# Performance work log

Measured on AMD Instinct MI355X. Metric: run time of the kernel, lower is better.

The kernel has to match this reference:

```python
import jax, jax.numpy as jnp
import numpy as np

# J2 (von Mises) plane-strain elastoplasticity with linear isotropic hardening
# (faithful stand-in for pyprnn's J2Material: elastic predictor + radial return,
#  committed history = plastic strain tensor + accumulated plastic strain).
E_MOD = 3130.0   # Young's modulus (epoxy, MPa)
NU = 0.37        # Poisson ratio
SIG_Y = 64.8     # initial yield stress
H_ISO = 300.0    # linear isotropic hardening modulus
MU = E_MOD / (2.0 * (1.0 + NU))
LAM = E_MOD * NU / ((1.0 + NU) * (1.0 - 2.0 * NU))


def j2_update(eps, eps_p, alpha):
    """eps: [P,3] (exx, eyy, gamma_xy engineering); eps_p: [P,4] (xx,yy,zz,xy tensorial);
    alpha: [P] accumulated plastic strain. Returns (stress [P,3], eps_p_new, alpha_new)."""
    ee_xx = eps[:, 0] - eps_p[:, 0]
    ee_yy = eps[:, 1] - eps_p[:, 1]
    ee_zz = -eps_p[:, 2]                      # plane strain: total ezz = 0
    ee_xy = 0.5 * eps[:, 2] - eps_p[:, 3]     # tensorial shear
    tr = ee_xx + ee_yy + ee_zz
    # trial (elastic predictor) stress
    sxx = LAM * tr + 2.0 * MU * ee_xx
    syy = LAM * tr + 2.0 * MU * ee_yy
    szz = LAM * tr + 2.0 * MU * ee_zz
    sxy = 2.0 * MU * ee_xy
    p = (sxx + syy + szz) / 3.0
    dxx, dyy, dzz = sxx - p, syy - p, szz - p
    q = jnp.sqrt(1.5 * (dxx * dxx + dyy * dyy + dzz * dzz + 2.0 * sxy * sxy))
    f = q - (SIG_Y + H_ISO * alpha)
    dgam = jnp.maximum(f, 0.0) / (3.0 * MU + H_ISO)   # radial return, closed form
    qs = jnp.maximum(q, 1e-12)
    nxx, nyy, nzz, nxy = 1.5 * dxx / qs, 1.5 * dyy / qs, 1.5 * dzz / qs, 1.5 * sxy / qs
    two_mu_dg = 2.0 * MU * dgam
    sig = jnp.stack([sxx - two_mu_dg * nxx, syy - two_mu_dg * nyy, sxy - two_mu_dg * nxy], axis=-1)
    eps_p_new = eps_p + dgam[:, None] * jnp.stack([nxx, nyy, nzz, nxy], axis=-1)
    alpha_new = alpha + dgam
    return sig, eps_p_new, alpha_new


def setup_inputs() -> dict:
    key = jax.random.key(0)
    k1, k2, k3 = jax.random.split(key, 3)
    B, T, F = 16384, 128, 3
    MATPTS = 16
    L, O = MATPTS * F, 3
    x = jax.random.normal(k1, (B, T, F), dtype=jnp.float32) * 0.02  # strain paths
    W1 = jax.random.normal(k2, (L, F), dtype=jnp.float32) * (1.0 / np.sqrt(F))
    W2 = jax.random.normal(k3, (O, L), dtype=jnp.float32) * (1.0 / np.sqrt(L))
    return {"x": x, "W1": W1, "W2": W2}


def reference(x, W1, W2):
    B, T, F = x.shape
    L = W1.shape[0]
    P = B * (L // F)                 # total material points = batch * mat_pts
    W2s = jax.nn.softplus(W2)        # SoftLayer: positive weights, no bias
    xt = jnp.swapaxes(x, 0, 1)       # [T, B, F]

    def step(carry, xi):
        eps_p, alpha = carry
        lat = xi @ W1.T                       # fc1 (no bias): [B, L]
        eps = lat.reshape(P, F)               # per-material-point strain
        sig, eps_p, alpha = j2_update(eps, eps_p, alpha)   # update + commit
        out = sig.reshape(B, L) @ W2s.T       # fc2 softplus-weighted linear
        return (eps_p, alpha), out

    carry0 = (jnp.zeros((P, 4), jnp.float32), jnp.zeros((P,), jnp.float32))
    _, ys = jax.lax.scan(step, carry0, xt)    # ys: [T, B, O]
    return jnp.swapaxes(ys, 0, 1)             # [B, T, O]
```

## Files before the change

kernel.cpp:

```cpp
#include <hip/hip_runtime.h>
#include <math.h>


#define BLOCK 256
#define BPB 32
#define TSTEPS 128
#define ROWF (TSTEPS * 3)
#define ROWP 388

typedef float v2 __attribute__((ext_vector_type(2)));

static __device__ __forceinline__ v2 vfma(v2 a, v2 b, v2 c) {
    return __builtin_elementwise_fma(a, b, c);
}
static __device__ __forceinline__ v2 vmax(v2 a, v2 b) {
    return __builtin_elementwise_max(a, b);
}

#define DPP_BFLY3(a, b, c)                                                       \
  asm volatile(                                                                  \
    "s_nop 1\n\t"                                                                \
    "v_add_f32_dpp %0, %0, %0 quad_perm:[1,0,3,2] row_mask:0xf bank_mask:0xf\n\t"\
    "v_add_f32_dpp %1, %1, %1 quad_perm:[1,0,3,2] row_mask:0xf bank_mask:0xf\n\t"\
    "v_add_f32_dpp %2, %2, %2 quad_perm:[1,0,3,2] row_mask:0xf bank_mask:0xf\n\t"\
    "v_add_f32_dpp %0, %0, %0 quad_perm:[2,3,0,1] row_mask:0xf bank_mask:0xf\n\t"\
    "v_add_f32_dpp %1, %1, %1 quad_perm:[2,3,0,1] row_mask:0xf bank_mask:0xf\n\t"\
    "v_add_f32_dpp %2, %2, %2 quad_perm:[2,3,0,1] row_mask:0xf bank_mask:0xf\n\t"\
    "v_add_f32_dpp %0, %0, %0 row_half_mirror row_mask:0xf bank_mask:0xf\n\t"    \
    "v_add_f32_dpp %1, %1, %1 row_half_mirror row_mask:0xf bank_mask:0xf\n\t"    \
    "v_add_f32_dpp %2, %2, %2 row_half_mirror row_mask:0xf bank_mask:0xf"        \
    : "+v"(a), "+v"(b), "+v"(c))

__global__ __launch_bounds__(BLOCK, 2)
void prnn_j2_kernel(const float* __restrict__ x,
                    const float* __restrict__ W1,
                    const float* __restrict__ W2,
                    float* __restrict__ out)
{
    constexpr float MU    = (float)(3130.0 / (2.0 * (1.0 + 0.37)));
    constexpr float LAM   = (float)(3130.0 * 0.37 / ((1.0 + 0.37) * (1.0 - 2.0 * 0.37)));
    constexpr float SIG_Y = 64.8f;
    constexpr float H_ISO = 300.0f;
    const float TWO_MU  = 2.0f * MU;
    const float K3MU    = 3.0f * MU;
    const float INV_DEN = 1.0f / (3.0f * MU + H_ISO);
    const float KBULK   = LAM + TWO_MU * (1.0f / 3.0f);
    const float C_Q2    = 6.0f * MU * MU;
    const v2 VTHIRD = {1.0f/3.0f, 1.0f/3.0f};
    const v2 VQMIN  = {1e-24f, 1e-24f};
    const v2 VZERO  = {0.0f, 0.0f};

    __shared__ float xs[BPB * ROWP + 12];

    const int tid = threadIdx.x;
    const int bl  = tid >> 3;
    const int l   = tid & 7;
    const int blockBase = blockIdx.x * (BPB * ROWF);

    {
        const float4* xg = (const float4*)(x + blockBase);
        for (int i4 = tid; i4 < BPB * ROWF / 4; i4 += BLOCK) {
            int b  = i4 / (ROWF / 4);
            int r4 = i4 - b * (ROWF / 4);
            ((float4*)(xs + b * ROWP))[r4] = xg[i4];
        }
    }

    const int pa = l, pb = l + 8;
    v2 w1p[3][3], w2p[3][3];
    #pragma unroll
    for (int c = 0; c < 3; ++c)
        #pragma unroll
        for (int f = 0; f < 3; ++f) {
            w1p[c][f].x = W1[(3 * pa + c) * 3 + f];
            w1p[c][f].y = W1[(3 * pb + c) * 3 + f];
        }
    #pragma unroll
    for (int o = 0; o < 3; ++o)
        #pragma unroll
        for (int c = 0; c < 3; ++c) {
            float wa = W2[o * 48 + 3 * pa + c];
            float wb = W2[o * 48 + 3 * pb + c];
            w2p[o][c].x = fmaxf(wa, 0.0f) + log1pf(expf(-fabsf(wa)));
            w2p[o][c].y = fmaxf(wb, 0.0f) + log1pf(expf(-fabsf(wb)));
        }

    __syncthreads();

    v2 p0 = VZERO, p1 = VZERO, p2 = VZERO, p3 = VZERO;
    v2 yld = {SIG_Y, SIG_Y};
    float* xrow = &xs[bl * ROWP];
    const float4* xv = (const float4*)xrow;

#define J2_STEP(x0_, x1_, x2_, wp_)                                          \
  {                                                                          \
    const float x0s = (x0_), x1s = (x1_), x2s = (x2_);                       \
    const v2 x0 = {x0s, x0s}, x1 = {x1s, x1s}, x2 = {x2s, x2s};              \
    const v2 e0 = vfma(w1p[0][0], x0, vfma(w1p[0][1], x1, w1p[0][2] * x2));  \
    const v2 e1 = vfma(w1p[1][0], x0, vfma(w1p[1][1], x1, w1p[1][2] * x2));  \
    const v2 e2 = vfma(w1p[2][0], x0, vfma(w1p[2][1], x1, w1p[2][2] * x2));  \
    const v2 ee_xx = e0 - p0;                                                \
    const v2 ee_yy = e1 - p1;                                                \
    const v2 ee_xy = 0.5f * e2 - p3;                                         \
    const v2 tr = (ee_xx + ee_yy) - p2;                                      \
    const v2 c3 = tr * VTHIRD;                                               \
    const v2 exd = ee_xx - c3;                                               \
    const v2 eyd = ee_yy - c3;                                               \
    const v2 ezd = -p2 - c3;                                                 \
    v2 u = exd * exd;                                                        \
    u = vfma(eyd, eyd, u);                                                   \
    u = vfma(ezd, ezd, u);                                                   \
    const v2 t2 = ee_xy * ee_xy;                                             \
    u = vfma(t2, (v2){2.0f, 2.0f}, u);                                       \
    const v2 q2 = vmax(C_Q2 * u, VQMIN);                                     \
    v2 rq;                                                                   \
    rq.x = __builtin_amdgcn_rsqf(q2.x);                                      \
    rq.y = __builtin_amdgcn_rsqf(q2.y);                                      \
    const v2 q = q2 * rq;                                                    \
    const v2 dgam = vmax(q - yld, VZERO) * INV_DEN;                          \
    yld = vfma((v2){H_ISO, H_ISO}, dgam, yld);                               \
    const v2 k   = (K3MU * dgam) * rq;                                       \
    const v2 omk = 1.0f - k;                                                 \
    const v2 pm  = KBULK * tr;                                               \
    const v2 s0 = vfma(TWO_MU * exd, omk, pm);                               \
    const v2 s1 = vfma(TWO_MU * eyd, omk, pm);                               \
    const v2 s2 = (TWO_MU * ee_xy) * omk;                                    \
    p0 = vfma(k, exd, p0);                                                   \
    p1 = vfma(k, eyd, p1);                                                   \
    p2 = vfma(k, ezd, p2);                                                   \
    p3 = vfma(k, ee_xy, p3);                                                 \
    v2 q0 = vfma(w2p[0][0], s0, vfma(w2p[0][1], s1, w2p[0][2] * s2));        \
    v2 q1 = vfma(w2p[1][0], s0, vfma(w2p[1][1], s1, w2p[1][2] * s2));        \
    v2 q2o = vfma(w2p[2][0], s0, vfma(w2p[2][1], s1, w2p[2][2] * s2));       \
    float o0 = q0.x + q0.y;                                                  \
    float o1 = q1.x + q1.y;                                                  \
    float o2 = q2o.x + q2o.y;                                                \
    DPP_BFLY3(o0, o1, o2);                                                   \
    if (l < 3) { (wp_)[l] = (l == 0) ? o0 : ((l == 1) ? o1 : o2); }          \
  }

    float4 A = xv[0], Bv = xv[1], Cv = xv[2];
    for (int tb = 0; tb < TSTEPS / 4; ++tb) {
        float4 An = xv[3 * tb + 3];
        float4 Bn = xv[3 * tb + 4];
        float4 Cn = xv[3 * tb + 5];

        float* wp = xrow + 12 * tb;
        J2_STEP(A.x,  A.y,  A.z,  wp + 0);
        J2_STEP(A.w,  Bv.x, Bv.y, wp + 3);
        J2_STEP(Bv.z, Bv.w, Cv.x, wp + 6);
        J2_STEP(Cv.y, Cv.z, Cv.w, wp + 9);

        A = An; Bv = Bn; Cv = Cn;
    }
#undef J2_STEP

    __syncthreads();

    {
        float4* og = (float4*)(out + blockBase);
        for (int i4 = tid; i4 < BPB * ROWF / 4; i4 += BLOCK) {
            int b  = i4 / (ROWF / 4);
            int r4 = i4 - b * (ROWF / 4);
            og[i4] = ((const float4*)(xs + b * ROWP))[r4];
        }
    }
}

extern "C" void kernel_launch(void* const* d_in, const int* in_sizes, int n_in,
                              void* d_out, int out_size, void* d_ws, size_t ws_size,
                              hipStream_t stream) {
    const float* x  = (const float*)d_in[0];
    const float* W1 = (const float*)d_in[1];
    const float* W2 = (const float*)d_in[2];
    float* out = (float*)d_out;

    const int B = 16384;
    dim3 grid(B / BPB);
    dim3 block(BLOCK);
    prnn_j2_kernel<<<grid, block, 0, stream>>>(x, W1, W2, out);
}
```

Before: 123.0 us.

## Process two batch rows per thread group to interleave independent J2 recurrences

Each 8-lane group now handles two batch rows at once, running two independent J2 time-step chains interleaved. The output reductions of both rows are merged into one six-value DPP butterfly, and the write is spread across lanes. Block size per batch doubles to 64 rows and launch bounds drop to one block per CU. The aim is more instruction-level parallelism to hide the latency of the serial recurrence. In exchange, register use per thread goes up, shared memory per block doubles, and there are half as many blocks, which may lower occupancy.

New measurement: 128.1 us. +4.1%, slower.

```diff
diff --git a/kernel.cpp b/kernel.cpp
--- a/kernel.cpp
+++ b/kernel.cpp
@@ -3,7 +3,7 @@
 
 
 #define BLOCK 256
-#define BPB 32
+#define BPB 64
 #define TSTEPS 128
 #define ROWF (TSTEPS * 3)
 #define ROWP 388
@@ -17,43 +17,96 @@
     return __builtin_elementwise_max(a, b);
 }
 
-#define DPP_BFLY3(a, b, c)                                                       \
+#define DPP_BFLY6(a, b, c, d, e, f)                                              \
   asm volatile(                                                                  \
     "s_nop 1\n\t"                                                                \
     "v_add_f32_dpp %0, %0, %0 quad_perm:[1,0,3,2] row_mask:0xf bank_mask:0xf\n\t"\
     "v_add_f32_dpp %1, %1, %1 quad_perm:[1,0,3,2] row_mask:0xf bank_mask:0xf\n\t"\
     "v_add_f32_dpp %2, %2, %2 quad_perm:[1,0,3,2] row_mask:0xf bank_mask:0xf\n\t"\
+    "v_add_f32_dpp %3, %3, %3 quad_perm:[1,0,3,2] row_mask:0xf bank_mask:0xf\n\t"\
+    "v_add_f32_dpp %4, %4, %4 quad_perm:[1,0,3,2] row_mask:0xf bank_mask:0xf\n\t"\
+    "v_add_f32_dpp %5, %5, %5 quad_perm:[1,0,3,2] row_mask:0xf bank_mask:0xf\n\t"\
     "v_add_f32_dpp %0, %0, %0 quad_perm:[2,3,0,1] row_mask:0xf bank_mask:0xf\n\t"\
     "v_add_f32_dpp %1, %1, %1 quad_perm:[2,3,0,1] row_mask:0xf bank_mask:0xf\n\t"\
     "v_add_f32_dpp %2, %2, %2 quad_perm:[2,3,0,1] row_mask:0xf bank_mask:0xf\n\t"\
+    "v_add_f32_dpp %3, %3, %3 quad_perm:[2,3,0,1] row_mask:0xf bank_mask:0xf\n\t"\
+    "v_add_f32_dpp %4, %4, %4 quad_perm:[2,3,0,1] row_mask:0xf bank_mask:0xf\n\t"\
+    "v_add_f32_dpp %5, %5, %5 quad_perm:[2,3,0,1] row_mask:0xf bank_mask:0xf\n\t"\
     "v_add_f32_dpp %0, %0, %0 row_half_mirror row_mask:0xf bank_mask:0xf\n\t"    \
     "v_add_f32_dpp %1, %1, %1 row_half_mirror row_mask:0xf bank_mask:0xf\n\t"    \
-    "v_add_f32_dpp %2, %2, %2 row_half_mirror row_mask:0xf bank_mask:0xf"        \
-    : "+v"(a), "+v"(b), "+v"(c))
-
-__global__ __launch_bounds__(BLOCK, 2)
-void prnn_j2_kernel(const float* __restrict__ x,
-                    const float* __restrict__ W1,
-                    const float* __restrict__ W2,
-                    float* __restrict__ out)
+    "v_add_f32_dpp %2, %2, %2 row_half_mirror row_mask:0xf bank_mask:0xf\n\t"    \
+    "v_add_f32_dpp %3, %3, %3 row_half_mirror row_mask:0xf bank_mask:0xf\n\t"    \
+    "v_add_f32_dpp %4, %4, %4 row_half_mirror row_mask:0xf bank_mask:0xf\n\t"    \
+    "v_add_f32_dpp %5, %5, %5 row_half_mirror row_mask:0xf bank_mask:0xf"        \
+    : "+v"(a), "+v"(b), "+v"(c), "+v"(d), "+v"(e), "+v"(f))
+
+struct St { v2 p0, p1, p2, p3, yld; };
+
+__device__ __forceinline__ void j2_step(const v2 (&w1p)[3][3], const v2 (&w2p)[3][3],
+                                        float x0s, float x1s, float x2s, St& S,
+                                        float& o0, float& o1, float& o2)
 {
     constexpr float MU    = (float)(3130.0 / (2.0 * (1.0 + 0.37)));
     constexpr float LAM   = (float)(3130.0 * 0.37 / ((1.0 + 0.37) * (1.0 - 2.0 * 0.37)));
-    constexpr float SIG_Y = 64.8f;
     constexpr float H_ISO = 300.0f;
     const float TWO_MU  = 2.0f * MU;
     const float K3MU    = 3.0f * MU;
     const float INV_DEN = 1.0f / (3.0f * MU + H_ISO);
     const float KBULK   = LAM + TWO_MU * (1.0f / 3.0f);
     const float C_Q2    = 6.0f * MU * MU;
-    const v2 VTHIRD = {1.0f/3.0f, 1.0f/3.0f};
-    const v2 VQMIN  = {1e-24f, 1e-24f};
-    const v2 VZERO  = {0.0f, 0.0f};
-
+
+    const v2 x0 = {x0s, x0s}, x1 = {x1s, x1s}, x2 = {x2s, x2s};
+    const v2 e0 = vfma(w1p[0][0], x0, vfma(w1p[0][1], x1, w1p[0][2] * x2));
+    const v2 e1 = vfma(w1p[1][0], x0, vfma(w1p[1][1], x1, w1p[1][2] * x2));
+    const v2 e2 = vfma(w1p[2][0], x0, vfma(w1p[2][1], x1, w1p[2][2] * x2));
+    const v2 ee_xx = e0 - S.p0;
+    const v2 ee_yy = e1 - S.p1;
+    const v2 ee_xy = 0.5f * e2 - S.p3;
+    const v2 tr = (ee_xx + ee_yy) - S.p2;
+    const v2 c3 = tr * (1.0f / 3.0f);
+    const v2 exd = ee_xx - c3;
+    const v2 eyd = ee_yy - c3;
+    const v2 ezd = -S.p2 - c3;
+    v2 u = exd * exd;
+    u = vfma(eyd, eyd, u);
+    u = vfma(ezd, ezd, u);
+    u = vfma(ee_xy * ee_xy, (v2){2.0f, 2.0f}, u);
+    const v2 q2 = vmax(C_Q2 * u, (v2){1e-24f, 1e-24f});
+    v2 rq;
+    rq.x = __builtin_amdgcn_rsqf(q2.x);
+    rq.y = __builtin_amdgcn_rsqf(q2.y);
+    const v2 q = q2 * rq;
+    const v2 dgam = vmax(q - S.yld, (v2){0.0f, 0.0f}) * INV_DEN;
+    S.yld = vfma((v2){H_ISO, H_ISO}, dgam, S.yld);
+    const v2 k   = (K3MU * dgam) * rq;
+    const v2 omk = 1.0f - k;
+    const v2 pm  = KBULK * tr;
+    const v2 s0 = vfma(TWO_MU * exd, omk, pm);
+    const v2 s1 = vfma(TWO_MU * eyd, omk, pm);
+    const v2 s2 = (TWO_MU * ee_xy) * omk;
+    S.p0 = vfma(k, exd, S.p0);
+    S.p1 = vfma(k, eyd, S.p1);
+    S.p2 = vfma(k, ezd, S.p2);
+    S.p3 = vfma(k, ee_xy, S.p3);
+    v2 r0 = vfma(w2p[0][0], s0, vfma(w2p[0][1], s1, w2p[0][2] * s2));
+    v2 r1 = vfma(w2p[1][0], s0, vfma(w2p[1][1], s1, w2p[1][2] * s2));
+    v2 r2 = vfma(w2p[2][0], s0, vfma(w2p[2][1], s1, w2p[2][2] * s2));
+    o0 = r0.x + r0.y;
+    o1 = r1.x + r1.y;
+    o2 = r2.x + r2.y;
+}
+
+__global__ __launch_bounds__(BLOCK, 1)
+void prnn_j2_kernel(const float* __restrict__ x,
+                    const float* __restrict__ W1,
+                    const float* __restrict__ W2,
+                    float* __restrict__ out)
+{
+    constexpr float SIG_Y = 64.8f;
     __shared__ float xs[BPB * ROWP + 12];
 
     const int tid = threadIdx.x;
-    const int bl  = tid >> 3;
+    const int g   = tid >> 3;
     const int l   = tid & 7;
     const int blockBase = blockIdx.x * (BPB * ROWF);
 
@@ -87,73 +140,51 @@
 
     __syncthreads();
 
-    v2 p0 = VZERO, p1 = VZERO, p2 = VZERO, p3 = VZERO;
-    v2 yld = {SIG_Y, SIG_Y};
-    float* xrow = &xs[bl * ROWP];
-    const float4* xv = (const float4*)xrow;
-
-#define J2_STEP(x0_, x1_, x2_, wp_)                                          \
+    St SA, SB;
+    SA.p0 = SA.p1 = SA.p2 = SA.p3 = (v2){0.f, 0.f};
+    SB.p0 = SB.p1 = SB.p2 = SB.p3 = (v2){0.f, 0.f};
+    SA.yld = SB.yld = (v2){SIG_Y, SIG_Y};
+
+    float* xrowA = &xs[(2 * g + 0) * ROWP];
+    float* xrowB = &xs[(2 * g + 1) * ROWP];
+    const float4* xvA = (const float4*)xrowA;
+    const float4* xvB = (const float4*)xrowB;
+
+    const int comp   = l & 3;
+    const bool wact  = comp < 3;
+    const bool isA   = l < 4;
+    float* wbase = (isA ? xrowA : xrowB) + comp;
+
+    float4 A0 = xvA[0], A1 = xvA[1], A2 = xvA[2];
+    float4 B0 = xvB[0], B1 = xvB[1], B2 = xvB[2];
+
+    for (int tb = 0; tb < TSTEPS / 4; ++tb) {
+        float4 An0 = xvA[3 * tb + 3], An1 = xvA[3 * tb + 4], An2 = xvA[3 * tb + 5];
+        float4 Bn0 = xvB[3 * tb + 3], Bn1 = xvB[3 * tb + 4], Bn2 = xvB[3 * tb + 5];
+
+        const int wo = 12 * tb;
+
+#define DO_STEP(ax, ay, az, bx, by, bz, j)                                   \
   {                                                                          \
-    const float x0s = (x0_), x1s = (x1_), x2s = (x2_);                       \
-    const v2 x0 = {x0s, x0s}, x1 = {x1s, x1s}, x2 = {x2s, x2s};              \
-    const v2 e0 = vfma(w1p[0][0], x0, vfma(w1p[0][1], x1, w1p[0][2] * x2));  \
-    const v2 e1 = vfma(w1p[1][0], x0, vfma(w1p[1][1], x1, w1p[1][2] * x2));  \
-    const v2 e2 = vfma(w1p[2][0], x0, vfma(w1p[2][1], x1, w1p[2][2] * x2));  \
-    const v2 ee_xx = e0 - p0;                                                \
-    const v2 ee_yy = e1 - p1;                                                \
-    const v2 ee_xy = 0.5f * e2 - p3;                                         \
-    const v2 tr = (ee_xx + ee_yy) - p2;                                      \
-    const v2 c3 = tr * VTHIRD;                                               \
-    const v2 exd = ee_xx - c3;                                               \
-    const v2 eyd = ee_yy - c3;                                               \
-    const v2 ezd = -p2 - c3;                                                 \
-    v2 u = exd * exd;                                                        \
-    u = vfma(eyd, eyd, u);                                                   \
-    u = vfma(ezd, ezd, u);                                                   \
-    const v2 t2 = ee_xy * ee_xy;                                             \
-    u = vfma(t2, (v2){2.0f, 2.0f}, u);                                       \
-    const v2 q2 = vmax(C_Q2 * u, VQMIN);                                     \
-    v2 rq;                                                                   \
-    rq.x = __builtin_amdgcn_rsqf(q2.x);                                      \
-    rq.y = __builtin_amdgcn_rsqf(q2.y);                                      \
-    const v2 q = q2 * rq;                                                    \
-    const v2 dgam = vmax(q - yld, VZERO) * INV_DEN;                          \
-    yld = vfma((v2){H_ISO, H_ISO}, dgam, yld);                               \
-    const v2 k   = (K3MU * dgam) * rq;                                       \
-    const v2 omk = 1.0f - k;                                                 \
-    const v2 pm  = KBULK * tr;                                               \
-    const v2 s0 = vfma(TWO_MU * exd, omk, pm);                               \
-    const v2 s1 = vfma(TWO_MU * eyd, omk, pm);                               \
-    const v2 s2 = (TWO_MU * ee_xy) * omk;                                    \
-    p0 = vfma(k, exd, p0);                                                   \
-    p1 = vfma(k, eyd, p1);                                                   \
-    p2 = vfma(k, ezd, p2);                                                   \
-    p3 = vfma(k, ee_xy, p3);                                                 \
-    v2 q0 = vfma(w2p[0][0], s0, vfma(w2p[0][1], s1, w2p[0][2] * s2));        \
-    v2 q1 = vfma(w2p[1][0], s0, vfma(w2p[1][1], s1, w2p[1][2] * s2));        \
-    v2 q2o = vfma(w2p[2][0], s0, vfma(w2p[2][1], s1, w2p[2][2] * s2));       \
-    float o0 = q0.x + q0.y;                                                  \
-    float o1 = q1.x + q1.y;                                                  \
-    float o2 = q2o.x + q2o.y;                                                \
-    DPP_BFLY3(o0, o1, o2);                                                   \
-    if (l < 3) { (wp_)[l] = (l == 0) ? o0 : ((l == 1) ? o1 : o2); }          \
+    float a0, a1, a2, b0, b1, b2;                                            \
+    j2_step(w1p, w2p, (ax), (ay), (az), SA, a0, a1, a2);                     \
+    j2_step(w1p, w2p, (bx), (by), (bz), SB, b0, b1, b2);                     \
+    DPP_BFLY6(a0, a1, a2, b0, b1, b2);                                       \
+    float vA = (comp == 0) ? a0 : ((comp == 1) ? a1 : a2);                   \
+    float vB = (comp == 0) ? b0 : ((comp == 1) ? b1 : b2);                   \
+    float val = isA ? vA : vB;                                               \
+    if (wact) wbase[wo + 3 * (j)] = val;                                     \
   }
 
-    float4 A = xv[0], Bv = xv[1], Cv = xv[2];
-    for (int tb = 0; tb < TSTEPS / 4; ++tb) {
-        float4 An = xv[3 * tb + 3];
-        float4 Bn = xv[3 * tb + 4];
-        float4 Cn = xv[3 * tb + 5];
-
-        float* wp = xrow + 12 * tb;
-        J2_STEP(A.x,  A.y,  A.z,  wp + 0);
-        J2_STEP(A.w,  Bv.x, Bv.y, wp + 3);
-        J2_STEP(Bv.z, Bv.w, Cv.x, wp + 6);
-        J2_STEP(Cv.y, Cv.z, Cv.w, wp + 9);
-
-        A = An; Bv = Bn; Cv = Cn;
+        DO_STEP(A0.x, A0.y, A0.z,  B0.x, B0.y, B0.z, 0);
+        DO_STEP(A0.w, A1.x, A1.y,  B0.w, B1.x, B1.y, 1);
+        DO_STEP(A1.z, A1.w, A2.x,  B1.z, B1.w, B2.x, 2);
+        DO_STEP(A2.y, A2.z, A2.w,  B2.y, B2.z, B2.w, 3);
+#undef DO_STEP
+
+        A0 = An0; A1 = An1; A2 = An2;
+        B0 = Bn0; B1 = Bn1; B2 = Bn2;
     }
-#undef J2_STEP
 
     __syncthreads();
 
```
